# Optimization experiments

Hardware: AMD Instinct MI355X
Metric: run time of the kernel (lower is better)

The kernel has to match this reference:

```python
import jax, jax.numpy as jnp
import numpy as np

CAPACITY_FACTOR = 1.25
AUX_W = 0.1
Z_W = 0.001


def setup_inputs() -> dict:
    key = jax.random.key(0)
    k0, k1, k2, k3 = jax.random.split(key, 4)
    B, T, C, E, H = 4, 2048, 896, 3, 3584
    x = jax.random.normal(k0, (B, T, C), dtype=jnp.float32)
    Wr = jax.random.normal(k1, (E, C), dtype=jnp.float32) * 0.02   # router Linear(C->E)
    W1 = jax.random.normal(k2, (E, H, C), dtype=jnp.float32) * 0.02  # per-expert Linear(C->H)
    W2 = jax.random.normal(k3, (E, C, H), dtype=jnp.float32) * 0.02  # per-expert Linear(H->C)
    return {"x": x, "Wr": Wr, "W1": W1, "W2": W2}


def reference(x, Wr, W1, W2):
    B, T, C = x.shape
    E = Wr.shape[0]
    N = B * T
    capacity = int(CAPACITY_FACTOR * N / E)  # static

    # --- router ---
    logits = jnp.einsum('btc,ec->bte', x, Wr)                      # [B,T,E]
    z_loss = Z_W * jnp.mean(jax.nn.logsumexp(logits, axis=-1) ** 2)
    probs = jax.nn.softmax(logits, axis=-1)
    pf = probs.reshape(N, E)
    expert_index = jnp.argmax(pf, axis=-1)                          # top-1
    mask = jax.nn.one_hot(expert_index, E, dtype=x.dtype)           # [N,E]

    # capacity-limited dispatch: per expert keep top-`capacity` tokens by router prob.
    # (When an expert has <= capacity tokens this keeps all of them, matching the
    #  torch reference's two branches.)
    scores = jnp.where(mask > 0, pf, -jnp.inf).T                    # [E,N]
    _, top_idx = jax.lax.top_k(scores, capacity)                    # [E,capacity]
    disp = jnp.zeros((E, N), dtype=x.dtype).at[jnp.arange(E)[:, None], top_idx].set(1.0)
    dispatch = (disp * mask.T).T                                    # [N,E], kills -inf picks

    gates = pf * dispatch
    gates = gates / (jnp.sum(gates, axis=-1, keepdims=True) + 1e-6)  # [N,E]

    aux_loss = AUX_W * jnp.sum(dispatch.mean(axis=0) * pf.mean(axis=0)) * E

    # --- experts (dense over tokens, gated combine; dropout in eval = identity) ---
    xf = x.reshape(N, C)
    h = jax.nn.gelu(jnp.einsum('nc,ehc->neh', xf, W1), approximate=False)  # [N,E,H]
    y = jnp.einsum('neh,ech->nec', h, W2)                                   # [N,E,C]
    out = xf + jnp.einsum('nec,ne->nc', y, gates)                           # residual + combine
    return out.reshape(B, T, C), aux_loss + z_loss
```

## Files before the change

### kernel.cpp

```cpp
#include <hip/hip_runtime.h>
#include <stdint.h>

#define B_ 4
#define T_ 2048
#define C_ 896
#define E_ 3
#define H_ 3584
#define N_ 8192

typedef __attribute__((ext_vector_type(8))) short short8;
typedef __attribute__((ext_vector_type(4))) float f32x4;

#define OFF_XB   ((size_t)0)
#define OFF_W1B  ((size_t)14680064)
#define OFF_W2B  ((size_t)33947648)
#define OFF_HB   ((size_t)53215232)
#define OFF_PERM ((size_t)111935488)
#define OFF_EID  ((size_t)112033792)
#define OFF_GATE ((size_t)112066560)
#define OFF_PBUF ((size_t)112099328)
#define OFF_LSE2 ((size_t)112197632)
#define OFF_CNT  ((size_t)112230400)
#define OFF_P    OFF_XB

static __device__ __forceinline__ unsigned short f2b(float f) {
  union { float f; unsigned u; } v; v.f = f;
  unsigned r = v.u + 0x7FFFu + ((v.u >> 16) & 1u);
  return (unsigned short)(r >> 16);
}

static __device__ __forceinline__ float gelu_fast(float v) {
  float u = 0.7978845608f * v * fmaf(0.044715f * v, v, 1.0f);
  u = fminf(u, 20.0f);
  float t = __expf(2.0f * u);
  return v * t * __builtin_amdgcn_rcpf(t + 1.0f);
}

static __device__ __forceinline__ int xcd_chunk(int lin, int total) {
  int q = total >> 3, r = total & 7;
  int xcd = lin & 7, idx = lin >> 3;
  return (xcd < r ? xcd * (q + 1) : r * (q + 1) + (xcd - r) * q) + idx;
}

static __device__ __forceinline__ void grp_decode(int t, int rt, int ncol, int RG, int CG,
                                                  int* rowt, int* colt) {
  const int fullbands = rt / RG;
  const int bandsz = RG * ncol;
  if (t < fullbands * bandsz) {
    int band = t / bandsz, tr = t % bandsz;
    int cg = tr / (CG * RG), r2 = tr % (CG * RG);
    *rowt = band * RG + r2 / CG;
    *colt = cg * CG + r2 % CG;
  } else {
    int t2 = t - fullbands * bandsz;
    int tail = rt - fullbands * RG;
    int cg = t2 / (CG * tail), r2 = t2 % (CG * tail);
    *rowt = fullbands * RG + r2 / CG;
    *colt = cg * CG + r2 % CG;
  }
}

__global__ __launch_bounds__(256) void cvt2_kernel(const float* __restrict__ a,
                                                   const float* __restrict__ b,
                                                   unsigned short* __restrict__ oa,
                                                   unsigned short* __restrict__ ob, int n4) {
  const int half = gridDim.x >> 1;
  const float* src = (blockIdx.x < half) ? a : b;
  unsigned short* dst = (blockIdx.x < half) ? oa : ob;
  const int bid = (blockIdx.x < half) ? blockIdx.x : blockIdx.x - half;
  const int stride = half * blockDim.x;
  for (int i = bid * blockDim.x + threadIdx.x; i < n4; i += stride) {
    float4 v = reinterpret_cast<const float4*>(src)[i];
    ushort4 o;
    o.x = f2b(v.x); o.y = f2b(v.y); o.z = f2b(v.z); o.w = f2b(v.w);
    reinterpret_cast<ushort4*>(dst)[i] = o;
  }
}

__global__ __launch_bounds__(256) void router_kernel(
    const float* __restrict__ x, const float* __restrict__ Wr,
    unsigned short* __restrict__ xb,
    int* __restrict__ eid, float* __restrict__ gate,
    float* __restrict__ pbuf, float* __restrict__ lse2) {
  const int tid = threadIdx.x;
  const int sub = tid & 31;
  const int n = blockIdx.x * 8 + (tid >> 5);
  const float4* xr = reinterpret_cast<const float4*>(x + (size_t)n * C_);
  ushort4* xw = reinterpret_cast<ushort4*>(xb + (size_t)n * C_);
  const float4* w0p = reinterpret_cast<const float4*>(Wr + 0 * C_);
  const float4* w1p = reinterpret_cast<const float4*>(Wr + 1 * C_);
  const float4* w2p = reinterpret_cast<const float4*>(Wr + 2 * C_);
  float s0 = 0.f, s1 = 0.f, s2 = 0.f;
#pragma unroll
  for (int j = 0; j < 7; ++j) {
    const int idx = sub + 32 * j;
    float4 v = xr[idx];
    ushort4 o;
    o.x = f2b(v.x); o.y = f2b(v.y); o.z = f2b(v.z); o.w = f2b(v.w);
    xw[idx] = o;
    float4 a = w0p[idx], b = w1p[idx], c = w2p[idx];
    s0 += v.x * a.x + v.y * a.y + v.z * a.z + v.w * a.w;
    s1 += v.x * b.x + v.y * b.y + v.z * b.z + v.w * b.w;
    s2 += v.x * c.x + v.y * c.y + v.z * c.z + v.w * c.w;
  }
#pragma unroll
  for (int off = 16; off > 0; off >>= 1) {
    s0 += __shfl_xor(s0, off);
    s1 += __shfl_xor(s1, off);
    s2 += __shfl_xor(s2, off);
  }
  if (sub == 0) {
    float m = fmaxf(s0, fmaxf(s1, s2));
    float e0 = expf(s0 - m), e1 = expf(s1 - m), e2 = expf(s2 - m);
    float sum = e0 + e1 + e2;
    float p0 = e0 / sum, p1 = e1 / sum, p2 = e2 / sum;
    int am = 0; float best = s0;
    if (s1 > best) { best = s1; am = 1; }
    if (s2 > best) { best = s2; am = 2; }
    float pa = (am == 0) ? p0 : ((am == 1) ? p1 : p2);
    eid[n] = am;
    gate[n] = pa / (pa + 1e-6f);
    pbuf[n * 3 + 0] = p0; pbuf[n * 3 + 1] = p1; pbuf[n * 3 + 2] = p2;
    float lse = m + logf(sum);
    lse2[n] = lse * lse;
  }
}

__global__ __launch_bounds__(1024) void scatter_kernel(const int* __restrict__ eid,
                                                       int* __restrict__ counts,
                                                       int* __restrict__ perm) {
  __shared__ int hist[E_];
  __shared__ int base[E_];
  const int t = threadIdx.x;
  const int n = blockIdx.x * 1024 + t;
  if (t < E_) hist[t] = 0;
  __syncthreads();
  int e = eid[n];
  int l = atomicAdd(&hist[e], 1);
  __syncthreads();
  if (t < E_) base[t] = atomicAdd(&counts[t], hist[t]);
  __syncthreads();
  perm[e * N_ + base[e] + l] = n;
}

#define STAGE_TILE(bufA, bufB)                                                          \
  do {                                                                                  \
    _Pragma("unroll")                                                                   \
    for (int i_ = 0; i_ < 4; ++i_) {                                                    \
      __builtin_amdgcn_global_load_lds(                                                 \
          (const __attribute__((address_space(1))) void*)pA_[i_],                       \
          (__attribute__((address_space(3))) void*)&(bufA)[(wv * 4 + i_) * 512], 16, 0, 0); \
    }                                                                                   \
    _Pragma("unroll")                                                                   \
    for (int i_ = 0; i_ < 4; ++i_) {                                                    \
      __builtin_amdgcn_global_load_lds(                                                 \
          (const __attribute__((address_space(1))) void*)pB_[i_],                       \
          (__attribute__((address_space(3))) void*)&(bufB)[(wv * 4 + i_) * 512], 16, 0, 0); \
    }                                                                                   \
    _Pragma("unroll")                                                                   \
    for (int i_ = 0; i_ < 4; ++i_) { pA_[i_] += 64; pB_[i_] += 64; }                    \
  } while (0)

#define COMPUTE_TILE(bufA, bufB)                                                        \
  do {                                                                                  \
    _Pragma("unroll")                                                                   \
    for (int kk = 0; kk < 2; ++kk) {                                                    \
      const int sl_ = ((kk * 4 + (lane >> 4)) ^ (lane & 7)) * 8;                        \
      short8 af[4], bfv[4];                                                             \
      _Pragma("unroll")                                                                 \
      for (int m = 0; m < 4; ++m) {                                                     \
        int row = wm * 64 + m * 16 + (lane & 15);                                       \
        af[m] = *reinterpret_cast<const short8*>(&(bufA)[row * 64 + sl_]);              \
      }                                                                                 \
      _Pragma("unroll")                                                                 \
      for (int nn = 0; nn < 4; ++nn) {                                                  \
        int row = wn * 64 + nn * 16 + (lane & 15);                                      \
        bfv[nn] = *reinterpret_cast<const short8*>(&(bufB)[row * 64 + sl_]);            \
      }                                                                                 \
      _Pragma("unroll")                                                                 \
      for (int m = 0; m < 4; ++m)                                                       \
        _Pragma("unroll")                                                               \
        for (int nn = 0; nn < 4; ++nn)                                                  \
          acc[m][nn] = __builtin_amdgcn_mfma_f32_16x16x32_bf16(af[m], bfv[nn], acc[m][nn], 0, 0, 0); \
    }                                                                                   \
  } while (0)

#define K_LOOP(NT)                                                                      \
  do {                                                                                  \
    for (int kt = 0; kt < (NT); ++kt) {                                                 \
      STAGE_TILE(shA, shB);                                                             \
      __syncthreads();                                                                  \
      COMPUTE_TILE(shA, shB);                                                           \
      __syncthreads();                                                                  \
    }                                                                                   \
  } while (0)

__global__ __launch_bounds__(256) void gemm1_kernel(
    const unsigned short* __restrict__ xb,
    const unsigned short* __restrict__ w1b,
    unsigned short* __restrict__ h,
    const int* __restrict__ perm, const int* __restrict__ counts) {
  const int c0 = counts[0], c1 = counts[1], c2 = counts[2];
  const int rt0 = (c0 + 127) >> 7, rt1 = (c1 + 127) >> 7, rt2 = (c2 + 127) >> 7;
  const int n0 = rt0 * 28, n1 = rt1 * 28, n2 = rt2 * 28;
  const int total = n0 + n1 + n2;
  const int lin = blockIdx.x;
  if (lin >= total) return;
  const int wgid = xcd_chunk(lin, total);
  int e, rem, rt_e, count;
  if (wgid < n0)            { e = 0; rem = wgid;           rt_e = rt0; count = c0; }
  else if (wgid < n0 + n1)  { e = 1; rem = wgid - n0;      rt_e = rt1; count = c1; }
  else                      { e = 2; rem = wgid - n0 - n1; rt_e = rt2; count = c2; }
  int rowt, colt;
  grp_decode(rem, rt_e, 28, 8, 7, &rowt, &colt);
  const int row0 = rowt * 128;
  const int col0 = colt * 128;
  const int tid = threadIdx.x, lane = tid & 63, wv = tid >> 6;
  const int wm = wv >> 1, wn = wv & 1;
  const int* permE = perm + e * N_;
  const unsigned short* w1e = w1b + (size_t)e * H_ * C_;

  __shared__ __align__(16) unsigned short shA[128 * 64];
  __shared__ __align__(16) unsigned short shB[128 * 64];

  f32x4 acc[4][4];
#pragma unroll
  for (int i = 0; i < 4; ++i)
#pragma unroll
    for (int j = 0; j < 4; ++j) acc[i][j] = (f32x4){0.f, 0.f, 0.f, 0.f};

  const int cc = (((lane & 7) ^ (lane >> 3))) * 8;
  const unsigned short* pA_[4];
  const unsigned short* pB_[4];
#pragma unroll
  for (int i = 0; i < 4; ++i) {
    int s = row0 + (wv * 4 + i) * 8 + (lane >> 3);
    if (s >= count) s = count - 1;
    pA_[i] = xb + (size_t)permE[s] * C_ + cc;
    int r = (wv * 4 + i) * 8 + (lane >> 3);
    pB_[i] = w1e + (size_t)(col0 + r) * C_ + cc;
  }

  K_LOOP(C_ / 64);

#pragma unroll
  for (int m = 0; m < 4; ++m) {
    int rbase = wm * 64 + m * 16 + (lane >> 4) * 4;
#pragma unroll
    for (int i = 0; i < 4; ++i) {
      int s = row0 + rbase + i;
      if (s < count) {
        int ntok = permE[s];
#pragma unroll
        for (int nn = 0; nn < 4; ++nn) {
          int col = col0 + wn * 64 + nn * 16 + (lane & 15);
          h[(size_t)ntok * H_ + col] = f2b(gelu_fast(acc[m][nn][i]));
        }
      }
    }
  }
}

__global__ __launch_bounds__(256) void gemm2_kernel(
    const unsigned short* __restrict__ h,
    const unsigned short* __restrict__ w2b,
    const float* __restrict__ x,
    const float* __restrict__ gate,
    float* __restrict__ out, float* __restrict__ P,
    const int* __restrict__ perm, const int* __restrict__ counts) {
  const int c0 = counts[0], c1 = counts[1], c2 = counts[2];
  const int rt0 = (c0 + 127) >> 7, rt1 = (c1 + 127) >> 7, rt2 = (c2 + 127) >> 7;
  const int n0 = rt0 * 14, n1 = rt1 * 14, n2 = rt2 * 14;
  const int total = n0 + n1 + n2;
  const int lin = blockIdx.x;
  if (lin >= total) return;
  const int wgid = xcd_chunk(lin, total);
  int e, rem, rt_e, count;
  if (wgid < n0)            { e = 0; rem = wgid;           rt_e = rt0; count = c0; }
  else if (wgid < n0 + n1)  { e = 1; rem = wgid - n0;      rt_e = rt1; count = c1; }
  else                      { e = 2; rem = wgid - n0 - n1; rt_e = rt2; count = c2; }
  int rowt, c14;
  grp_decode(rem, rt_e, 14, 4, 7, &rowt, &c14);
  const int ks = c14 / 7;
  const int colt = c14 % 7;
  const int row0 = rowt * 128;
  const int col0 = colt * 128;
  const int kbase = ks * (H_ / 2);
  const int tid = threadIdx.x, lane = tid & 63, wv = tid >> 6;
  const int wm = wv >> 1, wn = wv & 1;
  const int* permE = perm + e * N_;
  const unsigned short* w2e = w2b + (size_t)e * C_ * H_;

  __shared__ __align__(16) unsigned short shA[128 * 64];
  __shared__ __align__(16) unsigned short shB[128 * 64];

  f32x4 acc[4][4];
#pragma unroll
  for (int i = 0; i < 4; ++i)
#pragma unroll
    for (int j = 0; j < 4; ++j) acc[i][j] = (f32x4){0.f, 0.f, 0.f, 0.f};

  const int cc = (((lane & 7) ^ (lane >> 3))) * 8;
  const unsigned short* pA_[4];
  const unsigned short* pB_[4];
#pragma unroll
  for (int i = 0; i < 4; ++i) {
    int s = row0 + (wv * 4 + i) * 8 + (lane >> 3);
    if (s >= count) s = count - 1;
    pA_[i] = h + (size_t)permE[s] * H_ + kbase + cc;
    int r = (wv * 4 + i) * 8 + (lane >> 3);
    pB_[i] = w2e + (size_t)(col0 + r) * H_ + kbase + cc;
  }

  K_LOOP((H_ / 2) / 64);

#pragma unroll
  for (int m = 0; m < 4; ++m) {
    int rbase = wm * 64 + m * 16 + (lane >> 4) * 4;
#pragma unroll
    for (int i = 0; i < 4; ++i) {
      int s = row0 + rbase + i;
      if (s < count) {
        int ntok = permE[s];
        float g = gate[ntok];
        if (ks == 0) {
#pragma unroll
          for (int nn = 0; nn < 4; ++nn) {
            int col = col0 + wn * 64 + nn * 16 + (lane & 15);
            out[(size_t)ntok * C_ + col] = x[(size_t)ntok * C_ + col] + g * acc[m][nn][i];
          }
        } else {
#pragma unroll
          for (int nn = 0; nn < 4; ++nn) {
            int col = col0 + wn * 64 + nn * 16 + (lane & 15);
            P[(size_t)ntok * C_ + col] = g * acc[m][nn][i];
          }
        }
      }
    }
  }
}

__global__ __launch_bounds__(256) void combine_kernel(
    float* __restrict__ out, const float* __restrict__ P, int n4,
    const float* __restrict__ lse2, const float* __restrict__ pbuf,
    const int* __restrict__ eid) {
  int stride = gridDim.x * blockDim.x;
  for (int i = blockIdx.x * blockDim.x + threadIdx.x; i < n4; i += stride) {
    float4 a = reinterpret_cast<float4*>(out)[i];
    float4 b = reinterpret_cast<const float4*>(P)[i];
    a.x += b.x; a.y += b.y; a.z += b.z; a.w += b.w;
    reinterpret_cast<float4*>(out)[i] = a;
  }
  if (blockIdx.x == 0) {
    __shared__ float sh[7][256];
    float a = 0.f, p0 = 0.f, p1 = 0.f, p2 = 0.f, c0 = 0.f, c1 = 0.f, c2 = 0.f;
    for (int n = threadIdx.x; n < N_; n += 256) {
      a += lse2[n];
      p0 += pbuf[n * 3 + 0]; p1 += pbuf[n * 3 + 1]; p2 += pbuf[n * 3 + 2];
      int e = eid[n];
      c0 += (e == 0); c1 += (e == 1); c2 += (e == 2);
    }
    sh[0][threadIdx.x] = a;
    sh[1][threadIdx.x] = p0; sh[2][threadIdx.x] = p1; sh[3][threadIdx.x] = p2;
    sh[4][threadIdx.x] = c0; sh[5][threadIdx.x] = c1; sh[6][threadIdx.x] = c2;
    for (int s = 128; s > 0; s >>= 1) {
      __syncthreads();
      if (threadIdx.x < (unsigned)s)
#pragma unroll
        for (int q = 0; q < 7; ++q) sh[q][threadIdx.x] += sh[q][threadIdx.x + s];
    }
    if (threadIdx.x == 0) {
      const float invN = 1.0f / (float)N_;
      float z = 0.001f * (sh[0][0] * invN);
      float aux = 0.1f * (float)E_ *
                  (sh[4][0] * invN * sh[1][0] * invN +
                   sh[5][0] * invN * sh[2][0] * invN +
                   sh[6][0] * invN * sh[3][0] * invN);
      out[(size_t)N_ * C_] = z + aux;
    }
  }
}

extern "C" void kernel_launch(void* const* d_in, const int* in_sizes, int n_in,
                              void* d_out, int out_size, void* d_ws, size_t ws_size,
                              hipStream_t stream) {
  const float* x  = (const float*)d_in[0];
  const float* Wr = (const float*)d_in[1];
  const float* W1 = (const float*)d_in[2];
  const float* W2 = (const float*)d_in[3];
  float* out = (float*)d_out;
  char* ws = (char*)d_ws;

  unsigned short* xb  = (unsigned short*)(ws + OFF_XB);
  unsigned short* w1b = (unsigned short*)(ws + OFF_W1B);
  unsigned short* w2b = (unsigned short*)(ws + OFF_W2B);
  unsigned short* hb  = (unsigned short*)(ws + OFF_HB);
  int*   perm  = (int*)(ws + OFF_PERM);
  int*   eid   = (int*)(ws + OFF_EID);
  float* gate  = (float*)(ws + OFF_GATE);
  float* pbuf  = (float*)(ws + OFF_PBUF);
  float* lse2  = (float*)(ws + OFF_LSE2);
  int*   counts = (int*)(ws + OFF_CNT);
  float* P     = (float*)(ws + OFF_P);

  hipMemsetAsync(counts, 0, E_ * sizeof(int), stream);

  cvt2_kernel<<<2048, 256, 0, stream>>>(W1, W2, w1b, w2b, E_ * H_ * C_ / 4);

  router_kernel<<<N_ / 8, 256, 0, stream>>>(x, Wr, xb, eid, gate, pbuf, lse2);
  scatter_kernel<<<N_ / 1024, 1024, 0, stream>>>(eid, counts, perm);

  gemm1_kernel<<<27 * 28 * E_, 256, 0, stream>>>(xb, w1b, hb, perm, counts);
  gemm2_kernel<<<27 * 14 * E_, 256, 0, stream>>>(hb, w2b, x, gate, out, P, perm, counts);
  combine_kernel<<<2048, 256, 0, stream>>>(out, P, N_ * C_ / 4, lse2, pbuf, eid);
}
```

Measured before the change: 218.7 us.

## Overlap weight bf16 conversion with router and gemm1 kernels

Removes the standalone cvt2 kernel. W1 conversion now runs in extra blocks of the router launch, and W2 conversion runs in 512 extra blocks prepended to the gemm1 launch. The aim is to hide the weight-conversion bandwidth cost behind other work and save a kernel launch. In exchange, the conversion blocks compete with the GEMM blocks for compute units and memory bandwidth. The GEMM tiles also start after the conversion blocks in dispatch order, which could delay them.

```diff
diff --git a/kernel.cpp b/kernel.cpp
--- a/kernel.cpp
+++ b/kernel.cpp
@@ -7,6 +7,7 @@
 #define E_ 3
 #define H_ 3584
 #define N_ 8192
+#define CVB 512
 
 typedef __attribute__((ext_vector_type(8))) short short8;
 typedef __attribute__((ext_vector_type(4))) float f32x4;
@@ -60,16 +61,11 @@
   }
 }
 
-__global__ __launch_bounds__(256) void cvt2_kernel(const float* __restrict__ a,
-                                                   const float* __restrict__ b,
-                                                   unsigned short* __restrict__ oa,
-                                                   unsigned short* __restrict__ ob, int n4) {
-  const int half = gridDim.x >> 1;
-  const float* src = (blockIdx.x < half) ? a : b;
-  unsigned short* dst = (blockIdx.x < half) ? oa : ob;
-  const int bid = (blockIdx.x < half) ? blockIdx.x : blockIdx.x - half;
-  const int stride = half * blockDim.x;
-  for (int i = bid * blockDim.x + threadIdx.x; i < n4; i += stride) {
+static __device__ __forceinline__ void cvt_stride(const float* __restrict__ src,
+                                                  unsigned short* __restrict__ dst,
+                                                  int n4, int bid, int nblk) {
+  const int stride = nblk * 256;
+  for (int i = bid * 256 + threadIdx.x; i < n4; i += stride) {
     float4 v = reinterpret_cast<const float4*>(src)[i];
     ushort4 o;
     o.x = f2b(v.x); o.y = f2b(v.y); o.z = f2b(v.z); o.w = f2b(v.w);
@@ -81,7 +77,12 @@
     const float* __restrict__ x, const float* __restrict__ Wr,
     unsigned short* __restrict__ xb,
     int* __restrict__ eid, float* __restrict__ gate,
-    float* __restrict__ pbuf, float* __restrict__ lse2) {
+    float* __restrict__ pbuf, float* __restrict__ lse2,
+    const float* __restrict__ W1, unsigned short* __restrict__ w1b) {
+  if (blockIdx.x >= N_ / 8) {
+    cvt_stride(W1, w1b, E_ * H_ * C_ / 4, blockIdx.x - N_ / 8, 1024);
+    return;
+  }
   const int tid = threadIdx.x;
   const int sub = tid & 31;
   const int n = blockIdx.x * 8 + (tid >> 5);
@@ -199,12 +200,17 @@
     const unsigned short* __restrict__ xb,
     const unsigned short* __restrict__ w1b,
     unsigned short* __restrict__ h,
-    const int* __restrict__ perm, const int* __restrict__ counts) {
+    const int* __restrict__ perm, const int* __restrict__ counts,
+    const float* __restrict__ W2, unsigned short* __restrict__ w2b) {
+  if (blockIdx.x < CVB) {
+    cvt_stride(W2, w2b, E_ * C_ * H_ / 4, blockIdx.x, CVB);
+    return;
+  }
   const int c0 = counts[0], c1 = counts[1], c2 = counts[2];
   const int rt0 = (c0 + 127) >> 7, rt1 = (c1 + 127) >> 7, rt2 = (c2 + 127) >> 7;
   const int n0 = rt0 * 28, n1 = rt1 * 28, n2 = rt2 * 28;
   const int total = n0 + n1 + n2;
-  const int lin = blockIdx.x;
+  const int lin = blockIdx.x - CVB;
   if (lin >= total) return;
   const int wgid = xcd_chunk(lin, total);
   int e, rem, rt_e, count;
@@ -406,12 +412,10 @@
 
   hipMemsetAsync(counts, 0, E_ * sizeof(int), stream);
 
-  cvt2_kernel<<<2048, 256, 0, stream>>>(W1, W2, w1b, w2b, E_ * H_ * C_ / 4);
-
-  router_kernel<<<N_ / 8, 256, 0, stream>>>(x, Wr, xb, eid, gate, pbuf, lse2);
+  router_kernel<<<2048, 256, 0, stream>>>(x, Wr, xb, eid, gate, pbuf, lse2, W1, w1b);
   scatter_kernel<<<N_ / 1024, 1024, 0, stream>>>(eid, counts, perm);
 
-  gemm1_kernel<<<27 * 28 * E_, 256, 0, stream>>>(xb, w1b, hb, perm, counts);
+  gemm1_kernel<<<CVB + 27 * 28 * E_, 256, 0, stream>>>(xb, w1b, hb, perm, counts, W2, w2b);
   gemm2_kernel<<<27 * 14 * E_, 256, 0, stream>>>(hb, w2b, x, gate, out, P, perm, counts);
   combine_kernel<<<2048, 256, 0, stream>>>(out, P, N_ * C_ / 4, lse2, pbuf, eid);
 }
```

After: 216.7 us. About the same (-0.9%).
